# Kernel tuning notes

Measured on AMD Instinct MI355X. Metric: run time of the kernel, lower is better.

## Reference

```python
import jax, jax.numpy as jnp
import numpy as np

N_HEADS = 8
D_TIME = 128
D_TGT = 128
D_KEYS = D_TIME // N_HEADS  # 16
LN_EPS = 1e-5


def _layer_norm(x, gamma, beta):
    mu = jnp.mean(x, axis=-1, keepdims=True)
    var = jnp.var(x, axis=-1, keepdims=True)
    return (x - mu) * jax.lax.rsqrt(var + LN_EPS) * gamma + beta


def setup_inputs() -> dict:
    key = jax.random.key(0)
    ks = jax.random.split(key, 16)
    B, N, L, D = 4, 207, 64, D_TIME
    s = 1.0 / np.sqrt(D)
    inp = {
        "time_features_Q": jax.random.normal(ks[0], (B, N, L, D), jnp.float32),
        "time_features_K": jax.random.normal(ks[1], (B, N, L, D), jnp.float32),
        "target_features_K": jax.random.normal(ks[2], (B, N, L, D_TGT), jnp.float32),
        # Linear weights stored as [in, out] (y = x @ W + b)
        "Wq": jax.random.normal(ks[3], (D, D), jnp.float32) * s,
        "bq": jnp.zeros((D,), jnp.float32),
        "Wk": jax.random.normal(ks[4], (D, D), jnp.float32) * s,
        "bk": jnp.zeros((D,), jnp.float32),
        "Wv": jax.random.normal(ks[5], (D, D), jnp.float32) * s,
        "bv": jnp.zeros((D,), jnp.float32),
        "Wot": jax.random.normal(ks[6], (D, D), jnp.float32) * s,
        "bot": jnp.zeros((D,), jnp.float32),
        "Wtg": jax.random.normal(ks[7], (D_TGT, D_TGT), jnp.float32) * s,
        "btg": jnp.zeros((D_TGT,), jnp.float32),
        "g_time": jnp.ones((D,), jnp.float32),
        "b_time": jnp.zeros((D,), jnp.float32),
        "g_tgt": jnp.ones((D_TGT,), jnp.float32),
        "b_tgt": jnp.zeros((D_TGT,), jnp.float32),
    }
    return inp


def reference(time_features_Q, time_features_K, target_features_K,
              Wq, bq, Wk, bk, Wv, bv, Wot, bot, Wtg, btg,
              g_time, b_time, g_tgt, b_tgt):
    B, N, Lq, D = time_features_Q.shape
    Lk = time_features_K.shape[2]
    H, dk = N_HEADS, D_KEYS

    def split_heads(x, d):
        # [B,N,L,H*d] -> [B,N,H,L,d]
        return x.reshape(B, N, -1, H, d).transpose(0, 1, 3, 2, 4)

    q = split_heads(time_features_Q @ Wq + bq, dk)
    k = split_heads(time_features_K @ Wk + bk, dk)
    v = split_heads(time_features_K @ Wv + bv, dk)

    # Unnormalized scores (no softmax), scaled by sqrt(d_keys)
    attn_score = jnp.einsum('bnhqd,bnhkd->bnhqk', q, k) / np.sqrt(dk)

    # Time branch: score @ values -> merge heads -> proj -> (dropout=eval noop) -> residual + LN
    tv = jnp.einsum('bnhqk,bnhkd->bnhqd', attn_score, v)
    tv = tv.transpose(0, 1, 3, 2, 4).reshape(B, N, Lq, D)
    tv = tv @ Wot + bot
    time_value = _layer_norm(tv + time_features_Q, g_time, b_time)

    # Target branch: reuse the same score tensor on raw target features
    Dt = target_features_K.shape[-1]
    tk = target_features_K.reshape(B, N, Lk, H, Dt // H).transpose(0, 1, 3, 2, 4)
    ct = jnp.einsum('bnhqk,bnhkd->bnhqd', attn_score, tk)
    ct = ct.transpose(0, 1, 3, 2, 4).reshape(B, N, Lq, Dt)
    ct = ct @ Wtg + btg
    cross_target = _layer_norm(ct, g_tgt, b_tgt)

    return attn_score, time_value, cross_target
```

## Files before the change

kernel.cpp:

```cpp
#include <hip/hip_runtime.h>

typedef float f32x4 __attribute__((ext_vector_type(4)));
typedef short s16x4 __attribute__((ext_vector_type(4)));
typedef short s16x8 __attribute__((ext_vector_type(8)));

__device__ __forceinline__ short f2bf(float f) {
    union { float f; unsigned u; } c; c.f = f;
    return (short)((c.u + 0x7FFFu + ((c.u >> 16) & 1u)) >> 16);
}

__device__ __forceinline__ int swz128(int row, int col) {
    return row * 128 + (col ^ ((row & 7) << 3));
}
__device__ __forceinline__ int swz64(int row, int col) {
    return row * 64 + (col ^ ((row & 7) << 3));
}

__global__ __launch_bounds__(256) void k_prep(
    const float* __restrict__ Wq, const float* __restrict__ Wk,
    const float* __restrict__ Wv, const float* __restrict__ Wot,
    const float* __restrict__ Wtg, short* __restrict__ Wt) {
    const float* srcs[5] = {Wq, Wk, Wv, Wot, Wtg};
    const float* W = srcs[blockIdx.x];
    short* dst = Wt + blockIdx.x * 16384;
    const int t = threadIdx.x;
#pragma unroll 4
    for (int i = 0; i < 64; ++i) {
        int idx = i * 256 + t;
        int k = idx >> 7, n = idx & 127;
        dst[n * 128 + k] = f2bf(W[idx]);
    }
}

__device__ __forceinline__ s16x8 wfrag(const short* __restrict__ Wt,
                                       int ni, int kk, int m, int quad) {
    return *(const s16x8*)(Wt + (ni * 16 + m) * 128 + kk * 32 + quad * 8);
}

__global__ __launch_bounds__(256, 2) void k_main(
    const float* __restrict__ XQ, const float* __restrict__ XK,
    const float* __restrict__ Tgt, const short* __restrict__ Wt,
    const float* __restrict__ bq, const float* __restrict__ bk,
    const float* __restrict__ bv, const float* __restrict__ bot,
    const float* __restrict__ btg,
    const float* __restrict__ g_time, const float* __restrict__ b_time,
    const float* __restrict__ g_tgt, const float* __restrict__ b_tgt,
    float* __restrict__ out0, float* __restrict__ out1, float* __restrict__ out2) {
    const int bn = blockIdx.x;
    const int t = threadIdx.x;
    const int w = t >> 6, lane = t & 63, m = lane & 15, quad = lane >> 4;
    const int r0 = w * 16;

    __shared__ short BQ[64 * 128];
    __shared__ short BK[64 * 128];
    __shared__ short BV[128 * 64];
    __shared__ short BT[128 * 64];
    __shared__ short BS[4][16 * 64];

    const size_t base = (size_t)bn * 8192;
    const short* Wqt = Wt;
    const short* Wkt = Wt + 16384;
    const short* Wvt = Wt + 32768;
    const short* Wot_t = Wt + 49152;
    const short* Wtg_t = Wt + 65536;
    short* myS = BS[w];

    {
        const float* sq = XQ + base;
        const float* sk = XK + base;
        const float* st = Tgt + base;
#pragma unroll
        for (int it = 0; it < 8; ++it) {
            int e = t + it * 256;
            int row = e >> 5, c4 = (e & 31) * 4;
            f32x4 xq = *(const f32x4*)(sq + e * 4);
            f32x4 xk = *(const f32x4*)(sk + e * 4);
            f32x4 xt = *(const f32x4*)(st + e * 4);
            s16x4 pq, pk;
#pragma unroll
            for (int r = 0; r < 4; ++r) { pq[r] = f2bf(xq[r]); pk[r] = f2bf(xk[r]); }
            *(s16x4*)(BQ + swz128(row, c4)) = pq;
            *(s16x4*)(BK + swz128(row, c4)) = pk;
#pragma unroll
            for (int r = 0; r < 4; ++r) BT[swz64(c4 + r, row)] = f2bf(xt[r]);
        }
    }
    __syncthreads();

    s16x8 qf[8];
    {
        s16x8 a[4];
#pragma unroll
        for (int kk = 0; kk < 4; ++kk)
            a[kk] = *(const s16x8*)(BQ + swz128(r0 + m, kk * 32 + quad * 8));
        f32x4 accq[8];
#pragma unroll
        for (int ni = 0; ni < 8; ++ni) {
            accq[ni] = (f32x4){0.f, 0.f, 0.f, 0.f};
#pragma unroll
            for (int kk = 0; kk < 4; ++kk)
                accq[ni] = __builtin_amdgcn_mfma_f32_16x16x32_bf16(
                    a[kk], wfrag(Wqt, ni, kk, m, quad), accq[ni], 0, 0, 0);
        }
#pragma unroll
        for (int ni = 0; ni < 8; ++ni) {
            const float bb = bq[ni * 16 + m];
#pragma unroll
            for (int r = 0; r < 4; ++r)
                BQ[swz128(r0 + quad * 4 + r, ni * 16 + m)] = f2bf(accq[ni][r] + bb);
        }
#pragma unroll
        for (int h = 0; h < 8; ++h) {
            qf[h] = (s16x8){0, 0, 0, 0, 0, 0, 0, 0};
            if (quad < 2)
                qf[h] = *(const s16x8*)(BQ + swz128(r0 + m, h * 16 + quad * 8));
        }
    }

    {
        s16x8 a[4];
#pragma unroll
        for (int kk = 0; kk < 4; ++kk)
            a[kk] = *(const s16x8*)(BK + swz128(r0 + m, kk * 32 + quad * 8));
        f32x4 acck[8], accv[8];
#pragma unroll
        for (int ni = 0; ni < 8; ++ni) {
            acck[ni] = (f32x4){0.f, 0.f, 0.f, 0.f};
            accv[ni] = (f32x4){0.f, 0.f, 0.f, 0.f};
#pragma unroll
            for (int kk = 0; kk < 4; ++kk) {
                acck[ni] = __builtin_amdgcn_mfma_f32_16x16x32_bf16(
                    a[kk], wfrag(Wkt, ni, kk, m, quad), acck[ni], 0, 0, 0);
                accv[ni] = __builtin_amdgcn_mfma_f32_16x16x32_bf16(
                    a[kk], wfrag(Wvt, ni, kk, m, quad), accv[ni], 0, 0, 0);
            }
        }
#pragma unroll
        for (int ni = 0; ni < 8; ++ni) {
            const float bbk = bk[ni * 16 + m];
            const float bbv = bv[ni * 16 + m];
#pragma unroll
            for (int r = 0; r < 4; ++r) {
                BK[swz128(r0 + quad * 4 + r, ni * 16 + m)] = f2bf(acck[ni][r] + bbk);
                BV[swz64(ni * 16 + m, r0 + quad * 4 + r)] = f2bf(accv[ni][r] + bbv);
            }
        }
    }
    __syncthreads();

    f32x4 accv8[8], acct8[8];
    const s16x8 zfrag = (s16x8){0, 0, 0, 0, 0, 0, 0, 0};
    float* o0 = out0 + (size_t)bn * 32768;
#pragma unroll
    for (int h = 0; h < 8; ++h) {
        const s16x8 aq = qf[h];
#pragma unroll
        for (int nj = 0; nj < 4; ++nj) {
            s16x8 bk_ = zfrag;
            if (quad < 2)
                bk_ = *(const s16x8*)(BK + swz128(nj * 16 + m, h * 16 + quad * 8));
            f32x4 s = __builtin_amdgcn_mfma_f32_16x16x32_bf16(
                aq, bk_, (f32x4){0.f, 0.f, 0.f, 0.f}, 0, 0, 0);
#pragma unroll
            for (int r = 0; r < 4; ++r) {
                const int row = r0 + quad * 4 + r;
                const float sval = s[r] * 0.25f;
                o0[h * 4096 + row * 64 + nj * 16 + m] = sval;
                myS[swz64(quad * 4 + r, nj * 16 + m)] = f2bf(sval);
            }
        }
        accv8[h] = (f32x4){0.f, 0.f, 0.f, 0.f};
        acct8[h] = (f32x4){0.f, 0.f, 0.f, 0.f};
#pragma unroll
        for (int kk = 0; kk < 2; ++kk) {
            s16x8 sa  = *(const s16x8*)(myS + swz64(m, kk * 32 + quad * 8));
            s16x8 bv_ = *(const s16x8*)(BV + swz64(h * 16 + m, kk * 32 + quad * 8));
            s16x8 bt_ = *(const s16x8*)(BT + swz64(h * 16 + m, kk * 32 + quad * 8));
            accv8[h] = __builtin_amdgcn_mfma_f32_16x16x32_bf16(sa, bv_, accv8[h], 0, 0, 0);
            acct8[h] = __builtin_amdgcn_mfma_f32_16x16x32_bf16(sa, bt_, acct8[h], 0, 0, 0);
        }
    }
    __syncthreads();

#pragma unroll
    for (int h = 0; h < 8; ++h) {
#pragma unroll
        for (int r = 0; r < 4; ++r) {
            const int row = r0 + quad * 4 + r;
            BQ[swz128(row, h * 16 + m)] = f2bf(accv8[h][r]);
            BK[swz128(row, h * 16 + m)] = f2bf(acct8[h][r]);
        }
    }

#pragma unroll
    for (int br = 0; br < 2; ++br) {
        const short* sA = br == 0 ? BQ : BK;
        const short* Wp = br == 0 ? Wot_t : Wtg_t;
        const float* bias = br == 0 ? bot : btg;
        const float* gam = br == 0 ? g_time : g_tgt;
        const float* bet = br == 0 ? b_time : b_tgt;
        float* outp = (br == 0 ? out1 : out2) + base;
        const float* resid = br == 0 ? XQ + base : nullptr;

        s16x8 a[4];
#pragma unroll
        for (int kk = 0; kk < 4; ++kk)
            a[kk] = *(const s16x8*)(sA + swz128(r0 + m, kk * 32 + quad * 8));
        f32x4 acc[8];
#pragma unroll
        for (int ni = 0; ni < 8; ++ni) {
            acc[ni] = (f32x4){0.f, 0.f, 0.f, 0.f};
#pragma unroll
            for (int kk = 0; kk < 4; ++kk)
                acc[ni] = __builtin_amdgcn_mfma_f32_16x16x32_bf16(
                    a[kk], wfrag(Wp, ni, kk, m, quad), acc[ni], 0, 0, 0);
        }
        float y[8][4];
        float s1[4] = {0.f, 0.f, 0.f, 0.f}, s2[4] = {0.f, 0.f, 0.f, 0.f};
#pragma unroll
        for (int ni = 0; ni < 8; ++ni) {
            const int col = ni * 16 + m;
            const float bb = bias[col];
#pragma unroll
            for (int r = 0; r < 4; ++r) {
                const int row = r0 + quad * 4 + r;
                float v = acc[ni][r] + bb;
                if (resid) v += resid[row * 128 + col];
                y[ni][r] = v;
                s1[r] += v;
                s2[r] += v * v;
            }
        }
#pragma unroll
        for (int mask = 1; mask < 16; mask <<= 1) {
#pragma unroll
            for (int r = 0; r < 4; ++r) {
                s1[r] += __shfl_xor(s1[r], mask, 64);
                s2[r] += __shfl_xor(s2[r], mask, 64);
            }
        }
        float mu[4], rstd[4];
#pragma unroll
        for (int r = 0; r < 4; ++r) {
            mu[r] = s1[r] * (1.0f / 128.0f);
            float var = s2[r] * (1.0f / 128.0f) - mu[r] * mu[r];
            rstd[r] = rsqrtf(var + 1e-5f);
        }
#pragma unroll
        for (int ni = 0; ni < 8; ++ni) {
            const int col = ni * 16 + m;
            const float g = gam[col], bb = bet[col];
#pragma unroll
            for (int r = 0; r < 4; ++r) {
                const int row = r0 + quad * 4 + r;
                outp[row * 128 + col] = (y[ni][r] - mu[r]) * rstd[r] * g + bb;
            }
        }
    }
}

extern "C" void kernel_launch(void* const* d_in, const int* in_sizes, int n_in,
                              void* d_out, int out_size, void* d_ws, size_t ws_size,
                              hipStream_t stream) {
    const float* XQ  = (const float*)d_in[0];
    const float* XK  = (const float*)d_in[1];
    const float* Tgt = (const float*)d_in[2];
    const float* Wq  = (const float*)d_in[3];
    const float* bq  = (const float*)d_in[4];
    const float* Wk  = (const float*)d_in[5];
    const float* bk  = (const float*)d_in[6];
    const float* Wv  = (const float*)d_in[7];
    const float* bv  = (const float*)d_in[8];
    const float* Wot = (const float*)d_in[9];
    const float* bot = (const float*)d_in[10];
    const float* Wtg = (const float*)d_in[11];
    const float* btg = (const float*)d_in[12];
    const float* g_time = (const float*)d_in[13];
    const float* b_time = (const float*)d_in[14];
    const float* g_tgt  = (const float*)d_in[15];
    const float* b_tgt  = (const float*)d_in[16];

    const int BN = in_sizes[0] / 8192;

    short* Wt = (short*)d_ws;

    float* out0 = (float*)d_out;
    float* out1 = out0 + (size_t)BN * 32768;
    float* out2 = out1 + (size_t)BN * 8192;

    k_prep<<<5, 256, 0, stream>>>(Wq, Wk, Wv, Wot, Wtg, Wt);
    k_main<<<BN, 256, 0, stream>>>(XQ, XK, Tgt, Wt, bq, bk, bv, bot, btg,
                                   g_time, b_time, g_tgt, b_tgt,
                                   out0, out1, out2);
}
```

Baseline: 355.4 us.

## Cut LDS footprint to two buffers and raise occupancy to four blocks per CU

Shared memory drops from four 16KB tiles to two reused buffers (B2/B3) plus the score scratch, so four blocks per CU fit, and launch bounds are raised to match. XK loading is deferred and overlapped with the Q projection. Target features are read straight from global memory into MFMA B-fragments instead of being staged transposed in LDS. The P@V and P@T results are packed to bf16 pairs in registers to save VGPRs, at the cost of an extra barrier, strided uncoalesced global reads of the target tensor, and possible spills under the tighter register budget.

```diff
diff --git a/kernel.cpp b/kernel.cpp
--- a/kernel.cpp
+++ b/kernel.cpp
@@ -7,6 +7,10 @@
 __device__ __forceinline__ short f2bf(float f) {
     union { float f; unsigned u; } c; c.f = f;
     return (short)((c.u + 0x7FFFu + ((c.u >> 16) & 1u)) >> 16);
+}
+__device__ __forceinline__ unsigned pack2(float lo, float hi) {
+    return (unsigned)(unsigned short)f2bf(lo) |
+           ((unsigned)(unsigned short)f2bf(hi) << 16);
 }
 
 __device__ __forceinline__ int swz128(int row, int col) {
@@ -37,7 +41,7 @@
     return *(const s16x8*)(Wt + (ni * 16 + m) * 128 + kk * 32 + quad * 8);
 }
 
-__global__ __launch_bounds__(256, 2) void k_main(
+__global__ __launch_bounds__(256, 4) void k_main(
     const float* __restrict__ XQ, const float* __restrict__ XK,
     const float* __restrict__ Tgt, const short* __restrict__ Wt,
     const float* __restrict__ bq, const float* __restrict__ bk,
@@ -51,10 +55,8 @@
     const int w = t >> 6, lane = t & 63, m = lane & 15, quad = lane >> 4;
     const int r0 = w * 16;
 
-    __shared__ short BQ[64 * 128];
-    __shared__ short BK[64 * 128];
-    __shared__ short BV[128 * 64];
-    __shared__ short BT[128 * 64];
+    __shared__ short B2[64 * 128];
+    __shared__ short B3[64 * 128];
     __shared__ short BS[4][16 * 64];
 
     const size_t base = (size_t)bn * 8192;
@@ -67,32 +69,31 @@
 
     {
         const float* sq = XQ + base;
-        const float* sk = XK + base;
-        const float* st = Tgt + base;
 #pragma unroll
         for (int it = 0; it < 8; ++it) {
             int e = t + it * 256;
             int row = e >> 5, c4 = (e & 31) * 4;
-            f32x4 xq = *(const f32x4*)(sq + e * 4);
-            f32x4 xk = *(const f32x4*)(sk + e * 4);
-            f32x4 xt = *(const f32x4*)(st + e * 4);
-            s16x4 pq, pk;
-#pragma unroll
-            for (int r = 0; r < 4; ++r) { pq[r] = f2bf(xq[r]); pk[r] = f2bf(xk[r]); }
-            *(s16x4*)(BQ + swz128(row, c4)) = pq;
-            *(s16x4*)(BK + swz128(row, c4)) = pk;
-#pragma unroll
-            for (int r = 0; r < 4; ++r) BT[swz64(c4 + r, row)] = f2bf(xt[r]);
+            f32x4 x = *(const f32x4*)(sq + e * 4);
+            s16x4 p;
+#pragma unroll
+            for (int r = 0; r < 4; ++r) p[r] = f2bf(x[r]);
+            *(s16x4*)(B3 + swz128(row, c4)) = p;
         }
     }
     __syncthreads();
 
     s16x8 qf[8];
     {
+        const float* sk = XK + base;
+        f32x4 xk[8];
+#pragma unroll
+        for (int it = 0; it < 8; ++it)
+            xk[it] = *(const f32x4*)(sk + (t + it * 256) * 4);
+
         s16x8 a[4];
 #pragma unroll
         for (int kk = 0; kk < 4; ++kk)
-            a[kk] = *(const s16x8*)(BQ + swz128(r0 + m, kk * 32 + quad * 8));
+            a[kk] = *(const s16x8*)(B3 + swz128(r0 + m, kk * 32 + quad * 8));
         f32x4 accq[8];
 #pragma unroll
         for (int ni = 0; ni < 8; ++ni) {
@@ -107,21 +108,31 @@
             const float bb = bq[ni * 16 + m];
 #pragma unroll
             for (int r = 0; r < 4; ++r)
-                BQ[swz128(r0 + quad * 4 + r, ni * 16 + m)] = f2bf(accq[ni][r] + bb);
+                B3[swz128(r0 + quad * 4 + r, ni * 16 + m)] = f2bf(accq[ni][r] + bb);
         }
 #pragma unroll
         for (int h = 0; h < 8; ++h) {
             qf[h] = (s16x8){0, 0, 0, 0, 0, 0, 0, 0};
             if (quad < 2)
-                qf[h] = *(const s16x8*)(BQ + swz128(r0 + m, h * 16 + quad * 8));
-        }
-    }
+                qf[h] = *(const s16x8*)(B3 + swz128(r0 + m, h * 16 + quad * 8));
+        }
+#pragma unroll
+        for (int it = 0; it < 8; ++it) {
+            int e = t + it * 256;
+            int row = e >> 5, c4 = (e & 31) * 4;
+            s16x4 p;
+#pragma unroll
+            for (int r = 0; r < 4; ++r) p[r] = f2bf(xk[it][r]);
+            *(s16x4*)(B2 + swz128(row, c4)) = p;
+        }
+    }
+    __syncthreads();
 
     {
         s16x8 a[4];
 #pragma unroll
         for (int kk = 0; kk < 4; ++kk)
-            a[kk] = *(const s16x8*)(BK + swz128(r0 + m, kk * 32 + quad * 8));
+            a[kk] = *(const s16x8*)(B2 + swz128(r0 + m, kk * 32 + quad * 8));
         f32x4 acck[8], accv[8];
 #pragma unroll
         for (int ni = 0; ni < 8; ++ni) {
@@ -141,24 +152,32 @@
             const float bbv = bv[ni * 16 + m];
 #pragma unroll
             for (int r = 0; r < 4; ++r) {
-                BK[swz128(r0 + quad * 4 + r, ni * 16 + m)] = f2bf(acck[ni][r] + bbk);
-                BV[swz64(ni * 16 + m, r0 + quad * 4 + r)] = f2bf(accv[ni][r] + bbv);
+                B2[swz128(r0 + quad * 4 + r, ni * 16 + m)] = f2bf(acck[ni][r] + bbk);
+                B3[swz64(ni * 16 + m, r0 + quad * 4 + r)] = f2bf(accv[ni][r] + bbv);
             }
         }
     }
     __syncthreads();
 
-    f32x4 accv8[8], acct8[8];
+    unsigned pv[8][2], pt[8][2];
     const s16x8 zfrag = (s16x8){0, 0, 0, 0, 0, 0, 0, 0};
     float* o0 = out0 + (size_t)bn * 32768;
 #pragma unroll
     for (int h = 0; h < 8; ++h) {
+        const float* tg = Tgt + base + h * 16 + m;
+        float tgv[16];
+#pragma unroll
+        for (int j = 0; j < 8; ++j) {
+            tgv[j]     = tg[(quad * 8 + j) * 128];
+            tgv[8 + j] = tg[(32 + quad * 8 + j) * 128];
+        }
+
         const s16x8 aq = qf[h];
 #pragma unroll
         for (int nj = 0; nj < 4; ++nj) {
             s16x8 bk_ = zfrag;
             if (quad < 2)
-                bk_ = *(const s16x8*)(BK + swz128(nj * 16 + m, h * 16 + quad * 8));
+                bk_ = *(const s16x8*)(B2 + swz128(nj * 16 + m, h * 16 + quad * 8));
             f32x4 s = __builtin_amdgcn_mfma_f32_16x16x32_bf16(
                 aq, bk_, (f32x4){0.f, 0.f, 0.f, 0.f}, 0, 0, 0);
 #pragma unroll
@@ -169,32 +188,42 @@
                 myS[swz64(quad * 4 + r, nj * 16 + m)] = f2bf(sval);
             }
         }
-        accv8[h] = (f32x4){0.f, 0.f, 0.f, 0.f};
-        acct8[h] = (f32x4){0.f, 0.f, 0.f, 0.f};
-#pragma unroll
-        for (int kk = 0; kk < 2; ++kk) {
-            s16x8 sa  = *(const s16x8*)(myS + swz64(m, kk * 32 + quad * 8));
-            s16x8 bv_ = *(const s16x8*)(BV + swz64(h * 16 + m, kk * 32 + quad * 8));
-            s16x8 bt_ = *(const s16x8*)(BT + swz64(h * 16 + m, kk * 32 + quad * 8));
-            accv8[h] = __builtin_amdgcn_mfma_f32_16x16x32_bf16(sa, bv_, accv8[h], 0, 0, 0);
-            acct8[h] = __builtin_amdgcn_mfma_f32_16x16x32_bf16(sa, bt_, acct8[h], 0, 0, 0);
-        }
+        s16x8 bt0, bt1;
+#pragma unroll
+        for (int j = 0; j < 8; ++j) { bt0[j] = f2bf(tgv[j]); bt1[j] = f2bf(tgv[8 + j]); }
+
+        f32x4 av = (f32x4){0.f, 0.f, 0.f, 0.f};
+        f32x4 at = (f32x4){0.f, 0.f, 0.f, 0.f};
+        {
+            s16x8 sa0 = *(const s16x8*)(myS + swz64(m, quad * 8));
+            s16x8 bv0 = *(const s16x8*)(B3 + swz64(h * 16 + m, quad * 8));
+            av = __builtin_amdgcn_mfma_f32_16x16x32_bf16(sa0, bv0, av, 0, 0, 0);
+            at = __builtin_amdgcn_mfma_f32_16x16x32_bf16(sa0, bt0, at, 0, 0, 0);
+            s16x8 sa1 = *(const s16x8*)(myS + swz64(m, 32 + quad * 8));
+            s16x8 bv1 = *(const s16x8*)(B3 + swz64(h * 16 + m, 32 + quad * 8));
+            av = __builtin_amdgcn_mfma_f32_16x16x32_bf16(sa1, bv1, av, 0, 0, 0);
+            at = __builtin_amdgcn_mfma_f32_16x16x32_bf16(sa1, bt1, at, 0, 0, 0);
+        }
+        pv[h][0] = pack2(av[0], av[1]); pv[h][1] = pack2(av[2], av[3]);
+        pt[h][0] = pack2(at[0], at[1]); pt[h][1] = pack2(at[2], at[3]);
     }
     __syncthreads();
 
 #pragma unroll
     for (int h = 0; h < 8; ++h) {
 #pragma unroll
-        for (int r = 0; r < 4; ++r) {
-            const int row = r0 + quad * 4 + r;
-            BQ[swz128(row, h * 16 + m)] = f2bf(accv8[h][r]);
-            BK[swz128(row, h * 16 + m)] = f2bf(acct8[h][r]);
+        for (int j = 0; j < 2; ++j) {
+            const int ra = r0 + quad * 4 + 2 * j, rb = ra + 1;
+            B3[swz128(ra, h * 16 + m)] = (short)(pv[h][j] & 0xffff);
+            B3[swz128(rb, h * 16 + m)] = (short)(pv[h][j] >> 16);
+            B2[swz128(ra, h * 16 + m)] = (short)(pt[h][j] & 0xffff);
+            B2[swz128(rb, h * 16 + m)] = (short)(pt[h][j] >> 16);
         }
     }
 
 #pragma unroll
     for (int br = 0; br < 2; ++br) {
-        const short* sA = br == 0 ? BQ : BK;
+        const short* sA = br == 0 ? B3 : B2;
         const short* Wp = br == 0 ? Wot_t : Wtg_t;
         const float* bias = br == 0 ? bot : btg;
         const float* gam = br == 0 ? g_time : g_tgt;
```

Result: slower. 388.4 us (+9.3%).
